# Kernel tuning notes

Hardware: AMD Instinct MI355X
Metric: run time of the kernel (lower is better)

The kernel has to match this reference:

```python
import jax, jax.numpy as jnp
import numpy as np

# Static problem configuration
NUM_GRAPHS = 64
NODES_PER_GRAPH = 2048          # divisible by OUT_H
NODE_EMB_DIM = 256              # divisible by OUT_W
COND_EMB_DIM = 64
OUT_H, OUT_W = 16, 8            # AdaptiveAvgPool2d output -> pooled dim H*W = 128
MLP_H = 256
BN_EPS = 1e-5


def setup_inputs() -> dict:
    key = jax.random.key(0)
    ks = jax.random.split(key, 8)
    N = NUM_GRAPHS * NODES_PER_GRAPH
    x = jax.random.normal(ks[0], (N, NODE_EMB_DIM), dtype=jnp.float32)
    # equal contiguous segments: node i belongs to graph i // NODES_PER_GRAPH
    batch = jnp.repeat(jnp.arange(NUM_GRAPHS, dtype=jnp.int64), NODES_PER_GRAPH)
    conditioner_z_ref = jax.random.normal(ks[1], (N, COND_EMB_DIM), dtype=jnp.float32)
    mlp_in = COND_EMB_DIM + OUT_H * OUT_W
    W1 = jax.random.normal(ks[2], (mlp_in, MLP_H), dtype=jnp.float32) / np.sqrt(mlp_in)
    b1 = jnp.zeros((MLP_H,), dtype=jnp.float32)
    gamma = jnp.ones((MLP_H,), dtype=jnp.float32)
    beta = jnp.zeros((MLP_H,), dtype=jnp.float32)
    W2 = jax.random.normal(ks[3], (MLP_H, 3), dtype=jnp.float32) / np.sqrt(MLP_H)
    b2 = jnp.zeros((3,), dtype=jnp.float32)
    return {"x": x, "batch": batch, "conditioner_z_ref": conditioner_z_ref,
            "W1": W1, "b1": b1, "gamma": gamma, "beta": beta, "W2": W2, "b2": b2}


def _adaptive_pool(x):
    # x: [N_total, D] with equal contiguous segments of NODES_PER_GRAPH rows per graph.
    # AdaptiveAvgPool2d((OUT_H, OUT_W)) on each [n, D] "image"; since n % OUT_H == 0
    # and D % OUT_W == 0 the adaptive bins are uniform -> exact reshape-mean.
    B = x.shape[0] // NODES_PER_GRAPH
    xg = x.reshape(B, OUT_H, NODES_PER_GRAPH // OUT_H, OUT_W, NODE_EMB_DIM // OUT_W)
    pooled = xg.mean(axis=(2, 4))                 # [B, OUT_H, OUT_W]
    return pooled.reshape(B, OUT_H * OUT_W)       # [B, H*W]


def reference(x, batch, conditioner_z_ref, W1, b1, gamma, beta, W2, b2):
    batch_pooled = _adaptive_pool(x)                          # [B, H*W]
    gathered = batch_pooled[batch]                            # [N, H*W]
    h = jnp.concatenate([conditioner_z_ref, gathered], axis=1)  # [N, cond + H*W]
    # Linear -> BatchNorm1d (training-mode batch stats, biased var) -> GELU (exact)
    h = h @ W1 + b1                                           # [N, MLP_H]
    mean = h.mean(axis=0)
    var = h.var(axis=0)
    h = (h - mean) * jax.lax.rsqrt(var + BN_EPS) * gamma + beta
    h = jax.nn.gelu(h, approximate=False)
    return h @ W2 + b2                                        # [N, 3]
```

## Files before the change

kernel.cpp:

```cpp
#include <hip/hip_runtime.h>
#include <math.h>

#define NG    64
#define NPG   2048
#define NTOT  (NG*NPG)
#define D     256
#define ZD    64
#define PD    128
#define MH    256

typedef __attribute__((ext_vector_type(8))) short bf16x8;
typedef __attribute__((ext_vector_type(4))) float f32x4;

__device__ __forceinline__ unsigned short f2bf(float f){
  unsigned u = __float_as_uint(f);
  unsigned r = u + 0x7FFFu + ((u >> 16) & 1u);
  return (unsigned short)(r >> 16);
}
__device__ __forceinline__ float bf2f(unsigned short s){
  return __uint_as_float(((unsigned)s) << 16);
}
__device__ __forceinline__ float gelu_f(float x){
  float t = 0.7978845608028654f * fmaf(0.044715f * x, x * x, x);
  float e = __expf(2.0f * t);
  float th = 1.0f - 2.0f / (e + 1.0f);
  return 0.5f * x * (1.0f + th);
}

__global__ void pool_kernel(const float* __restrict__ x, float* __restrict__ pooled){
  int b  = blockIdx.x >> 4;
  int oh = blockIdx.x & 15;
  int tid = threadIdx.x;
  int c4 = tid & 63;
  int rq = tid >> 6;
  const float4* x4 = (const float4*)x;
  size_t base = (size_t)(b * NPG + oh * 128) * 64;
  float4 acc = make_float4(0.f, 0.f, 0.f, 0.f);
  #pragma unroll 8
  for (int i = 0; i < 32; i++){
    float4 v = x4[base + (size_t)(rq + i * 4) * 64 + c4];
    acc.x += v.x; acc.y += v.y; acc.z += v.z; acc.w += v.w;
  }
  __shared__ float red[256];
  red[tid] = acc.x + acc.y + acc.z + acc.w;
  __syncthreads();
  if (tid < 8){
    float s = 0.f;
    #pragma unroll
    for (int w = 0; w < 4; w++)
      #pragma unroll
      for (int j = 0; j < 8; j++)
        s += red[w * 64 + tid * 8 + j];
    pooled[b * PD + oh * 8 + tid] = s * (1.0f / 4096.0f);
  }
}

__launch_bounds__(256, 1)
__global__ void zstat_kernel(const float* __restrict__ z, float* __restrict__ St,
                             float* __restrict__ Cpart){
  __shared__ __align__(16) unsigned short zt[64 * 264];
  __shared__ float Cred[4][4096];
  int tid = threadIdx.x;
  int lane = tid & 63, wave = tid >> 6;
  int col = lane & 15, quad = lane >> 4;
  int g = blockIdx.x >> 1;
  int half = blockIdx.x & 1;
  const float4* z4 = (const float4*)z + ((size_t)g * 2048 + half * 1024) * 16;
  int d4 = tid & 15;

  f32x4 acc[4][4];
  #pragma unroll
  for (int a = 0; a < 4; a++)
    #pragma unroll
    for (int b = 0; b < 4; b++) acc[a][b] = (f32x4)(0.f);
  float s0 = 0.f, s1 = 0.f, s2 = 0.f, s3 = 0.f;

  for (int ch = 0; ch < 4; ch++){
    #pragma unroll
    for (int i = 0; i < 16; i++){
      int idx = tid + i * 256;
      int m = idx >> 4;
      float4 v = z4[ch * 4096 + idx];
      s0 += v.x; s1 += v.y; s2 += v.z; s3 += v.w;
      zt[(d4 * 4 + 0) * 264 + m] = f2bf(v.x);
      zt[(d4 * 4 + 1) * 264 + m] = f2bf(v.y);
      zt[(d4 * 4 + 2) * 264 + m] = f2bf(v.z);
      zt[(d4 * 4 + 3) * 264 + m] = f2bf(v.w);
    }
    __syncthreads();
    #pragma unroll
    for (int ks = 0; ks < 2; ks++){
      int k0 = wave * 64 + ks * 32;
      bf16x8 fr[4];
      #pragma unroll
      for (int t = 0; t < 4; t++)
        fr[t] = *(const bf16x8*)&zt[(t * 16 + col) * 264 + k0 + quad * 8];
      #pragma unroll
      for (int mt = 0; mt < 4; mt++)
        #pragma unroll
        for (int nt = 0; nt < 4; nt++)
          acc[mt][nt] = __builtin_amdgcn_mfma_f32_16x16x32_bf16(fr[mt], fr[nt], acc[mt][nt], 0, 0, 0);
    }
    __syncthreads();
  }

  s0 += __shfl_xor(s0, 16); s0 += __shfl_xor(s0, 32);
  s1 += __shfl_xor(s1, 16); s1 += __shfl_xor(s1, 32);
  s2 += __shfl_xor(s2, 16); s2 += __shfl_xor(s2, 32);
  s3 += __shfl_xor(s3, 16); s3 += __shfl_xor(s3, 32);
  if (quad == 0){
    atomicAdd(&St[(d4 * 4 + 0) * 64 + g], s0);
    atomicAdd(&St[(d4 * 4 + 1) * 64 + g], s1);
    atomicAdd(&St[(d4 * 4 + 2) * 64 + g], s2);
    atomicAdd(&St[(d4 * 4 + 3) * 64 + g], s3);
  }

  #pragma unroll
  for (int mt = 0; mt < 4; mt++)
    #pragma unroll
    for (int nt = 0; nt < 4; nt++)
      #pragma unroll
      for (int r = 0; r < 4; r++){
        int p = mt * 16 + quad * 4 + r;
        int q = nt * 16 + col;
        Cred[wave][p * 64 + q] = acc[mt][nt][r];
      }
  __syncthreads();
  float* dst = Cpart + (size_t)blockIdx.x * 4096;
  for (int f = tid; f < 4096; f += 256)
    dst[f] = Cred[0][f] + Cred[1][f] + Cred[2][f] + Cred[3][f];
}

__global__ void creduce_kernel(const float* __restrict__ Cpart, float* __restrict__ C){
  int o = blockIdx.x * 256 + threadIdx.x;
  float s = 0.f;
  #pragma unroll 8
  for (int b = 0; b < 128; b++) s += Cpart[(size_t)b * 4096 + o];
  C[o] = s;
}

__global__ void gmat_kernel(const float* __restrict__ pooled, const float* __restrict__ W1,
                            const float* __restrict__ b1, float* __restrict__ G){
  int b = blockIdx.x; int j = threadIdx.x;
  __shared__ float p[PD];
  if (j < PD) p[j] = pooled[b * PD + j];
  __syncthreads();
  float s = b1[j];
  #pragma unroll 8
  for (int k = 0; k < PD; k++) s = fmaf(p[k], W1[(size_t)(ZD + k) * MH + j], s);
  G[b * MH + j] = s;
}

__global__ void stats_kernel(const float* __restrict__ C, const float* __restrict__ St,
                             const float* __restrict__ G, const float* __restrict__ W1,
                             const float* __restrict__ gamma, const float* __restrict__ beta,
                             float* __restrict__ a_out, float* __restrict__ cprime){
  int j = blockIdx.x * 4 + (threadIdx.x >> 6);
  int p = threadIdx.x & 63;
  float wl = W1[(size_t)p * MH + j];
  float t1 = 0.f, t2 = 0.f;
  #pragma unroll
  for (int q = 0; q < 64; q++){
    float wq = __uint_as_float(__builtin_amdgcn_readlane(__float_as_uint(wl), q));
    t1 = fmaf(C [q * 64 + p], wq, t1);
    t2 = fmaf(St[q * 64 + p], wq, t2);
  }
  float g = G[p * MH + j];
  float v_wcw = wl * t1;
  float v_gs  = g * t2;
  float v_s   = t2;
  float v_g   = g;
  float v_g2  = g * g;
  #pragma unroll
  for (int off = 32; off; off >>= 1){
    v_wcw += __shfl_xor(v_wcw, off);
    v_gs  += __shfl_xor(v_gs , off);
    v_s   += __shfl_xor(v_s  , off);
    v_g   += __shfl_xor(v_g  , off);
    v_g2  += __shfl_xor(v_g2 , off);
  }
  const float invN = 1.0f / (float)NTOT;
  float mean = v_s * invN + v_g * (1.0f / 64.0f);
  float eh2  = v_wcw * invN + 2.0f * invN * v_gs + v_g2 * (1.0f / 64.0f);
  float var  = eh2 - mean * mean;
  float aj = gamma[j] * rsqrtf(var + 1e-5f);
  if (p == 0) a_out[j] = aj;
  cprime[p * MH + j] = fmaf(aj, g, beta[j] - aj * mean);
}

__launch_bounds__(256, 2)
__global__ void final_kernel(const float* __restrict__ z, const float* __restrict__ W1,
                             const float* __restrict__ Aj, const float* __restrict__ cp,
                             const float* __restrict__ W2, const float* __restrict__ b2,
                             float* __restrict__ out){
  __shared__ __align__(16) unsigned short zt[128 * 136];
  __shared__ __align__(16) unsigned short Wt[256 * 72];
  __shared__ float slab[2][384];
  int tid = threadIdx.x;
  int n0 = blockIdx.x * 128;
  int g = blockIdx.x >> 4;

  const float4* W14 = (const float4*)W1;
  #pragma unroll
  for (int i = 0; i < 16; i++){
    int idx = tid + i * 256;
    int k = idx >> 6, j4 = idx & 63;
    float4 v = W14[k * 64 + j4];
    Wt[(j4 * 4 + 0) * 72 + k] = f2bf(v.x);
    Wt[(j4 * 4 + 1) * 72 + k] = f2bf(v.y);
    Wt[(j4 * 4 + 2) * 72 + k] = f2bf(v.z);
    Wt[(j4 * 4 + 3) * 72 + k] = f2bf(v.w);
  }
  const float4* z4 = (const float4*)z + (size_t)n0 * 16;
  #pragma unroll
  for (int i = 0; i < 8; i++){
    int idx = tid + i * 256;
    int m = idx >> 4, d4 = idx & 15;
    float4 v = z4[idx];
    ushort4 h, l;
    h.x = f2bf(v.x); l.x = f2bf(v.x - bf2f(h.x));
    h.y = f2bf(v.y); l.y = f2bf(v.y - bf2f(h.y));
    h.z = f2bf(v.z); l.z = f2bf(v.z - bf2f(h.z));
    h.w = f2bf(v.w); l.w = f2bf(v.w - bf2f(h.w));
    *(ushort4*)&zt[m * 136 + d4 * 4]      = h;
    *(ushort4*)&zt[m * 136 + 64 + d4 * 4] = l;
  }
  __syncthreads();

  int lane = tid & 63, wave = tid >> 6;
  int wm = wave & 1, wn = wave >> 1;
  int col = lane & 15, quad = lane >> 4;
  int mbase = wm * 64, nbase = wn * 128;

  f32x4 acc[4][8];
  #pragma unroll
  for (int mt = 0; mt < 4; mt++)
    #pragma unroll
    for (int nt = 0; nt < 8; nt++) acc[mt][nt] = (f32x4)(0.f);

  #pragma unroll
  for (int ks = 0; ks < 4; ks++){
    int k0 = ks * 32;
    bf16x8 af[4], bfr[8];
    #pragma unroll
    for (int mt = 0; mt < 4; mt++)
      af[mt] = *(const bf16x8*)&zt[(mbase + mt * 16 + col) * 136 + k0 + quad * 8];
    #pragma unroll
    for (int nt = 0; nt < 8; nt++)
      bfr[nt] = *(const bf16x8*)&Wt[(nbase + nt * 16 + col) * 72 + (k0 & 63) + quad * 8];
    #pragma unroll
    for (int mt = 0; mt < 4; mt++)
      #pragma unroll
      for (int nt = 0; nt < 8; nt++)
        acc[mt][nt] = __builtin_amdgcn_mfma_f32_16x16x32_bf16(af[mt], bfr[nt], acc[mt][nt], 0, 0, 0);
  }

  float aj[8], cj[8], w2a[8], w2b[8], w2c[8];
  #pragma unroll
  for (int nt = 0; nt < 8; nt++){
    int j = nbase + nt * 16 + col;
    aj[nt] = Aj[j];
    cj[nt] = cp[g * MH + j];
    w2a[nt] = W2[j * 3 + 0];
    w2b[nt] = W2[j * 3 + 1];
    w2c[nt] = W2[j * 3 + 2];
  }

  #pragma unroll
  for (int mt = 0; mt < 4; mt++){
    #pragma unroll
    for (int r = 0; r < 4; r++){
      float o0 = 0.f, o1 = 0.f, o2 = 0.f;
      #pragma unroll
      for (int nt = 0; nt < 8; nt++){
        float h  = fmaf(aj[nt], acc[mt][nt][r], cj[nt]);
        float ge = gelu_f(h);
        o0 = fmaf(ge, w2a[nt], o0);
        o1 = fmaf(ge, w2b[nt], o1);
        o2 = fmaf(ge, w2c[nt], o2);
      }
      #pragma unroll
      for (int off = 8; off; off >>= 1){
        o0 += __shfl_xor(o0, off);
        o1 += __shfl_xor(o1, off);
        o2 += __shfl_xor(o2, off);
      }
      if (col == 0){
        int node = mbase + mt * 16 + quad * 4 + r;
        slab[wn][node * 3 + 0] = o0;
        slab[wn][node * 3 + 1] = o1;
        slab[wn][node * 3 + 2] = o2;
      }
    }
  }
  __syncthreads();
  float b2v[3] = {b2[0], b2[1], b2[2]};
  for (int f = tid; f < 384; f += 256)
    out[(size_t)blockIdx.x * 384 + f] = slab[0][f] + slab[1][f] + b2v[f % 3];
}

extern "C" void kernel_launch(void* const* d_in, const int* in_sizes, int n_in,
                              void* d_out, int out_size, void* d_ws, size_t ws_size,
                              hipStream_t stream){
  (void)in_sizes; (void)n_in; (void)out_size; (void)ws_size;
  const float* x     = (const float*)d_in[0];
  const float* z     = (const float*)d_in[2];
  const float* W1    = (const float*)d_in[3];
  const float* b1    = (const float*)d_in[4];
  const float* gamma = (const float*)d_in[5];
  const float* beta  = (const float*)d_in[6];
  const float* W2    = (const float*)d_in[7];
  const float* b2    = (const float*)d_in[8];
  float* out = (float*)d_out;

  float* W = (float*)d_ws;
  float* pooled = W;
  float* St     = W + 8192;
  float* C      = W + 12288;
  float* G      = W + 16384;
  float* Aj     = W + 32768;
  float* CP     = W + 33024;
  float* Cpart  = W + 49408;

  hipMemsetAsync((char*)d_ws + 8192 * 4, 0, 4096 * 4, stream);

  pool_kernel   <<<dim3(NG * 16),   dim3(256), 0, stream>>>(x, pooled);
  zstat_kernel  <<<dim3(128),       dim3(256), 0, stream>>>(z, St, Cpart);
  creduce_kernel<<<dim3(16),        dim3(256), 0, stream>>>(Cpart, C);
  gmat_kernel   <<<dim3(NG),        dim3(256), 0, stream>>>(pooled, W1, b1, G);
  stats_kernel  <<<dim3(64),        dim3(256), 0, stream>>>(C, St, G, W1, gamma, beta, Aj, CP);
  final_kernel  <<<dim3(NTOT / 128), dim3(256), 0, stream>>>(z, W1, Aj, CP, W2, b2, out);
}
```

Baseline: 311.1 us.

## Fuse pool and z-stats kernels, merge stats, precompute bf16 W1 once

```diff
diff --git a/kernel.cpp b/kernel.cpp
--- a/kernel.cpp
+++ b/kernel.cpp
@@ -4,7 +4,6 @@
 #define NG    64
 #define NPG   2048
 #define NTOT  (NG*NPG)
-#define D     256
 #define ZD    64
 #define PD    128
 #define MH    256
@@ -27,45 +26,47 @@
   return 0.5f * x * (1.0f + th);
 }
 
-__global__ void pool_kernel(const float* __restrict__ x, float* __restrict__ pooled){
-  int b  = blockIdx.x >> 4;
-  int oh = blockIdx.x & 15;
+__launch_bounds__(256)
+__global__ void k1_pool_zstat(const float* __restrict__ x, const float* __restrict__ z,
+                              float* __restrict__ pooled, float* __restrict__ St,
+                              float* __restrict__ C){
+  __shared__ __align__(16) unsigned short s_zt[64 * 264];
+  __shared__ float s_cred[4096];
   int tid = threadIdx.x;
-  int c4 = tid & 63;
-  int rq = tid >> 6;
-  const float4* x4 = (const float4*)x;
-  size_t base = (size_t)(b * NPG + oh * 128) * 64;
-  float4 acc = make_float4(0.f, 0.f, 0.f, 0.f);
-  #pragma unroll 8
-  for (int i = 0; i < 32; i++){
-    float4 v = x4[base + (size_t)(rq + i * 4) * 64 + c4];
-    acc.x += v.x; acc.y += v.y; acc.z += v.z; acc.w += v.w;
-  }
-  __shared__ float red[256];
-  red[tid] = acc.x + acc.y + acc.z + acc.w;
-  __syncthreads();
-  if (tid < 8){
-    float s = 0.f;
-    #pragma unroll
-    for (int w = 0; w < 4; w++)
-      #pragma unroll
-      for (int j = 0; j < 8; j++)
-        s += red[w * 64 + tid * 8 + j];
-    pooled[b * PD + oh * 8 + tid] = s * (1.0f / 4096.0f);
-  }
-}
-
-__launch_bounds__(256, 1)
-__global__ void zstat_kernel(const float* __restrict__ z, float* __restrict__ St,
-                             float* __restrict__ Cpart){
-  __shared__ __align__(16) unsigned short zt[64 * 264];
-  __shared__ float Cred[4][4096];
-  int tid = threadIdx.x;
+
+  if (blockIdx.x >= 256){
+    int bi = blockIdx.x - 256;
+    int b  = bi >> 4;
+    int oh = bi & 15;
+    int c4 = tid & 63;
+    int rq = tid >> 6;
+    const float4* x4 = (const float4*)x;
+    size_t base = (size_t)(b * NPG + oh * 128) * 64;
+    float4 acc = make_float4(0.f, 0.f, 0.f, 0.f);
+    #pragma unroll 8
+    for (int i = 0; i < 32; i++){
+      float4 v = x4[base + (size_t)(rq + i * 4) * 64 + c4];
+      acc.x += v.x; acc.y += v.y; acc.z += v.z; acc.w += v.w;
+    }
+    s_cred[tid] = acc.x + acc.y + acc.z + acc.w;
+    __syncthreads();
+    if (tid < 8){
+      float s = 0.f;
+      #pragma unroll
+      for (int w = 0; w < 4; w++)
+        #pragma unroll
+        for (int j = 0; j < 8; j++)
+          s += s_cred[w * 64 + tid * 8 + j];
+      pooled[b * PD + oh * 8 + tid] = s * (1.0f / 4096.0f);
+    }
+    return;
+  }
+
+  int blk = blockIdx.x;
+  int g = blk >> 2, q4 = blk & 3;
   int lane = tid & 63, wave = tid >> 6;
   int col = lane & 15, quad = lane >> 4;
-  int g = blockIdx.x >> 1;
-  int half = blockIdx.x & 1;
-  const float4* z4 = (const float4*)z + ((size_t)g * 2048 + half * 1024) * 16;
+  const float4* z4 = (const float4*)z + ((size_t)g * 2048 + q4 * 512) * 16;
   int d4 = tid & 15;
 
   f32x4 acc[4][4];
@@ -75,17 +76,17 @@
     for (int b = 0; b < 4; b++) acc[a][b] = (f32x4)(0.f);
   float s0 = 0.f, s1 = 0.f, s2 = 0.f, s3 = 0.f;
 
-  for (int ch = 0; ch < 4; ch++){
+  for (int ch = 0; ch < 2; ch++){
     #pragma unroll
     for (int i = 0; i < 16; i++){
       int idx = tid + i * 256;
       int m = idx >> 4;
       float4 v = z4[ch * 4096 + idx];
       s0 += v.x; s1 += v.y; s2 += v.z; s3 += v.w;
-      zt[(d4 * 4 + 0) * 264 + m] = f2bf(v.x);
-      zt[(d4 * 4 + 1) * 264 + m] = f2bf(v.y);
-      zt[(d4 * 4 + 2) * 264 + m] = f2bf(v.z);
-      zt[(d4 * 4 + 3) * 264 + m] = f2bf(v.w);
+      s_zt[(d4 * 4 + 0) * 264 + m] = f2bf(v.x);
+      s_zt[(d4 * 4 + 1) * 264 + m] = f2bf(v.y);
+      s_zt[(d4 * 4 + 2) * 264 + m] = f2bf(v.z);
+      s_zt[(d4 * 4 + 3) * 264 + m] = f2bf(v.w);
     }
     __syncthreads();
     #pragma unroll
@@ -94,7 +95,7 @@
       bf16x8 fr[4];
       #pragma unroll
       for (int t = 0; t < 4; t++)
-        fr[t] = *(const bf16x8*)&zt[(t * 16 + col) * 264 + k0 + quad * 8];
+        fr[t] = *(const bf16x8*)&s_zt[(t * 16 + col) * 264 + k0 + quad * 8];
       #pragma unroll
       for (int mt = 0; mt < 4; mt++)
         #pragma unroll
@@ -116,56 +117,56 @@
   }
 
   #pragma unroll
-  for (int mt = 0; mt < 4; mt++)
-    #pragma unroll
-    for (int nt = 0; nt < 4; nt++)
-      #pragma unroll
-      for (int r = 0; r < 4; r++){
-        int p = mt * 16 + quad * 4 + r;
-        int q = nt * 16 + col;
-        Cred[wave][p * 64 + q] = acc[mt][nt][r];
-      }
+  for (int w = 0; w < 4; w++){
+    if (wave == w){
+      #pragma unroll
+      for (int mt = 0; mt < 4; mt++)
+        #pragma unroll
+        for (int nt = 0; nt < 4; nt++)
+          #pragma unroll
+          for (int r = 0; r < 4; r++){
+            int p = mt * 16 + quad * 4 + r;
+            int qc = nt * 16 + col;
+            if (w == 0) s_cred[p * 64 + qc]  = acc[mt][nt][r];
+            else        s_cred[p * 64 + qc] += acc[mt][nt][r];
+          }
+    }
+    __syncthreads();
+  }
+  for (int f = tid; f < 4096; f += 256)
+    atomicAdd(&C[f], s_cred[f]);
+}
+
+__launch_bounds__(256)
+__global__ void k2_stats(const float* __restrict__ pooled, const float* __restrict__ W1,
+                         const float* __restrict__ b1, const float* __restrict__ gamma,
+                         const float* __restrict__ beta, const float* __restrict__ C,
+                         const float* __restrict__ St, float* __restrict__ Aj,
+                         float* __restrict__ cprime, unsigned short* __restrict__ Wbf){
+  __shared__ float pl[64 * 129];
+  int tid = threadIdx.x;
+  int jc = tid >> 6, lane = tid & 63;
+  int j = blockIdx.x * 4 + jc;
+
+  Wbf[(size_t)j * 64 + lane] = f2bf(W1[(size_t)lane * 256 + j]);
+
+  for (int idx = tid; idx < 8192; idx += 256)
+    pl[(idx >> 7) * 129 + (idx & 127)] = pooled[idx];
   __syncthreads();
-  float* dst = Cpart + (size_t)blockIdx.x * 4096;
-  for (int f = tid; f < 4096; f += 256)
-    dst[f] = Cred[0][f] + Cred[1][f] + Cred[2][f] + Cred[3][f];
-}
-
-__global__ void creduce_kernel(const float* __restrict__ Cpart, float* __restrict__ C){
-  int o = blockIdx.x * 256 + threadIdx.x;
-  float s = 0.f;
+
+  float g = b1[j];
   #pragma unroll 8
-  for (int b = 0; b < 128; b++) s += Cpart[(size_t)b * 4096 + o];
-  C[o] = s;
-}
-
-__global__ void gmat_kernel(const float* __restrict__ pooled, const float* __restrict__ W1,
-                            const float* __restrict__ b1, float* __restrict__ G){
-  int b = blockIdx.x; int j = threadIdx.x;
-  __shared__ float p[PD];
-  if (j < PD) p[j] = pooled[b * PD + j];
-  __syncthreads();
-  float s = b1[j];
-  #pragma unroll 8
-  for (int k = 0; k < PD; k++) s = fmaf(p[k], W1[(size_t)(ZD + k) * MH + j], s);
-  G[b * MH + j] = s;
-}
-
-__global__ void stats_kernel(const float* __restrict__ C, const float* __restrict__ St,
-                             const float* __restrict__ G, const float* __restrict__ W1,
-                             const float* __restrict__ gamma, const float* __restrict__ beta,
-                             float* __restrict__ a_out, float* __restrict__ cprime){
-  int j = blockIdx.x * 4 + (threadIdx.x >> 6);
-  int p = threadIdx.x & 63;
-  float wl = W1[(size_t)p * MH + j];
+  for (int k = 0; k < 128; k++)
+    g = fmaf(pl[lane * 129 + k], W1[(size_t)(ZD + k) * MH + j], g);
+
+  float wl = W1[(size_t)lane * MH + j];
   float t1 = 0.f, t2 = 0.f;
   #pragma unroll
   for (int q = 0; q < 64; q++){
     float wq = __uint_as_float(__builtin_amdgcn_readlane(__float_as_uint(wl), q));
-    t1 = fmaf(C [q * 64 + p], wq, t1);
-    t2 = fmaf(St[q * 64 + p], wq, t2);
-  }
-  float g = G[p * MH + j];
+    t1 = fmaf(C [q * 64 + lane], wq, t1);
+    t2 = fmaf(St[q * 64 + lane], wq, t2);
+  }
   float v_wcw = wl * t1;
   float v_gs  = g * t2;
   float v_s   = t2;
@@ -184,33 +185,21 @@
   float eh2  = v_wcw * invN + 2.0f * invN * v_gs + v_g2 * (1.0f / 64.0f);
   float var  = eh2 - mean * mean;
   float aj = gamma[j] * rsqrtf(var + 1e-5f);
-  if (p == 0) a_out[j] = aj;
-  cprime[p * MH + j] = fmaf(aj, g, beta[j] - aj * mean);
+  if (lane == 0) Aj[j] = aj;
+  cprime[lane * MH + j] = fmaf(aj, g, beta[j] - aj * mean);
 }
 
 __launch_bounds__(256, 2)
-__global__ void final_kernel(const float* __restrict__ z, const float* __restrict__ W1,
+__global__ void final_kernel(const float* __restrict__ z, const unsigned short* __restrict__ Wbf,
                              const float* __restrict__ Aj, const float* __restrict__ cp,
                              const float* __restrict__ W2, const float* __restrict__ b2,
                              float* __restrict__ out){
   __shared__ __align__(16) unsigned short zt[128 * 136];
-  __shared__ __align__(16) unsigned short Wt[256 * 72];
   __shared__ float slab[2][384];
   int tid = threadIdx.x;
   int n0 = blockIdx.x * 128;
   int g = blockIdx.x >> 4;
 
-  const float4* W14 = (const float4*)W1;
-  #pragma unroll
-  for (int i = 0; i < 16; i++){
-    int idx = tid + i * 256;
-    int k = idx >> 6, j4 = idx & 63;
-    float4 v = W14[k * 64 + j4];
-    Wt[(j4 * 4 + 0) * 72 + k] = f2bf(v.x);
-    Wt[(j4 * 4 + 1) * 72 + k] = f2bf(v.y);
-    Wt[(j4 * 4 + 2) * 72 + k] = f2bf(v.z);
-    Wt[(j4 * 4 + 3) * 72 + k] = f2bf(v.w);
-  }
   const float4* z4 = (const float4*)z + (size_t)n0 * 16;
   #pragma unroll
   for (int i = 0; i < 8; i++){
@@ -241,18 +230,17 @@
   #pragma unroll
   for (int ks = 0; ks < 4; ks++){
     int k0 = ks * 32;
-    bf16x8 af[4], bfr[8];
+    bf16x8 af[4];
     #pragma unroll
     for (int mt = 0; mt < 4; mt++)
       af[mt] = *(const bf16x8*)&zt[(mbase + mt * 16 + col) * 136 + k0 + quad * 8];
     #pragma unroll
-    for (int nt = 0; nt < 8; nt++)
-      bfr[nt] = *(const bf16x8*)&Wt[(nbase + nt * 16 + col) * 72 + (k0 & 63) + quad * 8];
-    #pragma unroll
-    for (int mt = 0; mt < 4; mt++)
-      #pragma unroll
-      for (int nt = 0; nt < 8; nt++)
-        acc[mt][nt] = __builtin_amdgcn_mfma_f32_16x16x32_bf16(af[mt], bfr[nt], acc[mt][nt], 0, 0, 0);
+    for (int nt = 0; nt < 8; nt++){
+      bf16x8 bv = *(const bf16x8*)&Wbf[(size_t)(nbase + nt * 16 + col) * 64 + (ks & 1) * 32 + quad * 8];
+      #pragma unroll
+      for (int mt = 0; mt < 4; mt++)
+        acc[mt][nt] = __builtin_amdgcn_mfma_f32_16x16x32_bf16(af[mt], bv, acc[mt][nt], 0, 0, 0);
+    }
   }
 
   float aj[8], cj[8], w2a[8], w2b[8], w2c[8];
@@ -317,17 +305,13 @@
   float* pooled = W;
   float* St     = W + 8192;
   float* C      = W + 12288;
-  float* G      = W + 16384;
-  float* Aj     = W + 32768;
-  float* CP     = W + 33024;
-  float* Cpart  = W + 49408;
-
-  hipMemsetAsync((char*)d_ws + 8192 * 4, 0, 4096 * 4, stream);
-
-  pool_kernel   <<<dim3(NG * 16),   dim3(256), 0, stream>>>(x, pooled);
-  zstat_kernel  <<<dim3(128),       dim3(256), 0, stream>>>(z, St, Cpart);
-  creduce_kernel<<<dim3(16),        dim3(256), 0, stream>>>(Cpart, C);
-  gmat_kernel   <<<dim3(NG),        dim3(256), 0, stream>>>(pooled, W1, b1, G);
-  stats_kernel  <<<dim3(64),        dim3(256), 0, stream>>>(C, St, G, W1, gamma, beta, Aj, CP);
-  final_kernel  <<<dim3(NTOT / 128), dim3(256), 0, stream>>>(z, W1, Aj, CP, W2, b2, out);
-}
+  float* Aj     = W + 16384;
+  float* CP     = W + 16640;
+  unsigned short* Wbf = (unsigned short*)(W + 33024);
+
+  hipMemsetAsync((char*)d_ws + 8192 * 4, 0, 8192 * 4, stream);
+
+  k1_pool_zstat<<<dim3(1280), dim3(256), 0, stream>>>(x, z, pooled, St, C);
+  k2_stats     <<<dim3(64),   dim3(256), 0, stream>>>(pooled, W1, b1, gamma, beta, C, St, Aj, CP, Wbf);
+  final_kernel <<<dim3(NTOT / 128), dim3(256), 0, stream>>>(z, Wbf, Aj, CP, W2, b2, out);
+}
```

Measured after the change: 282.5 us. -9.2%, faster.
